# Kernel tuning notes

Measured on AMD Instinct MI355X. Metric: run time of the kernel, lower is better.

Reference implementation:

```python
import jax, jax.numpy as jnp
import numpy as np


def setup_inputs() -> dict:
    key = jax.random.key(0)
    ks = jax.random.split(key, 8)
    B, S, H, I = 2, 1025, 3200, 12800
    T = B * S
    # int8 tensors represented as int32, symmetric range [-128, 126]
    hidden_states = jax.random.randint(ks[0], (B, S, H), 0, 255, dtype=jnp.int32) - 127
    scale_in = (jax.random.uniform(ks[1], (T,)) * 0.02 + 1e-4).astype(jnp.float16)
    w1 = jax.random.randint(ks[2], (I, H), 0, 255, dtype=jnp.int32) - 127
    w1_scale = (jax.random.uniform(ks[3], (I,)) * 0.01 + 1e-4).astype(jnp.float32)
    b1 = (jax.random.normal(ks[4], (I,)) * 0.02).astype(jnp.float16)
    w2 = jax.random.randint(ks[5], (H, I), 0, 255, dtype=jnp.int32) - 127
    w2_scale = (jax.random.uniform(ks[6], (H,)) * 0.01 + 1e-4).astype(jnp.float32)
    b2 = (jax.random.normal(ks[7], (H,)) * 0.02).astype(jnp.float16)
    return {"hidden_states": hidden_states, "scale_in": scale_in,
            "w1": w1, "w1_scale": w1_scale, "b1": b1,
            "w2": w2, "w2_scale": w2_scale, "b2": b2}


def _w8a8_linear(x_int, scale_x, w_int, w_scale, bias):
    # int8 GEMM with int32 accumulation, dequant with per-token * per-channel scales
    acc = jnp.matmul(x_int, w_int.T)  # [T, out] int32
    out = acc.astype(jnp.float32) * scale_x[:, None].astype(jnp.float32) * w_scale[None, :]
    return (out + bias.astype(jnp.float32)).astype(jnp.float16)


def _gelu_and_quant(x_f16):
    # fused GELU + per-token dynamic symmetric int8 quantization
    g = jax.nn.gelu(x_f16.astype(jnp.float32), approximate=False)  # [T, I]
    amax = jnp.max(jnp.abs(g), axis=-1)                              # [T]
    scale_act = (amax / 127.0).astype(jnp.float16)
    s = jnp.maximum(scale_act.astype(jnp.float32), 1e-8)
    q = jnp.clip(jnp.round(g / s[:, None]), -128, 127).astype(jnp.int32)
    return q, scale_act


def reference(hidden_states, scale_in, w1, w1_scale, b1, w2, w2_scale, b2):
    B, S, H = hidden_states.shape
    x = hidden_states.reshape(-1, H)               # [T, H] int
    fc1_out = _w8a8_linear(x, scale_in, w1, w1_scale, b1)      # [T, I] fp16
    act_out, scale_act = _gelu_and_quant(fc1_out)              # int8-as-int32, [T] fp16
    fc2_out = _w8a8_linear(act_out, scale_act, w2, w2_scale, b2)  # [T, H] fp16
    return fc2_out
```

## Files before the change

### kernel.cpp

```cpp
#include <hip/hip_runtime.h>
#include <hip/hip_fp16.h>

typedef int v4i __attribute__((ext_vector_type(4)));

#define AS1C(p) ((const __attribute__((address_space(1))) void*)(p))
#define AS3(p)  ((__attribute__((address_space(3))) void*)(p))
#define BARRIER() do { __builtin_amdgcn_s_barrier(); asm volatile("" ::: "memory"); } while (0)

template <int EPI, int BM>
__launch_bounds__(256, 2)
__global__ void gemm_p2(const signed char* __restrict__ A, const signed char* __restrict__ Bw,
                        int M, int N, int K,
                        const float* __restrict__ scale_tok, const float* __restrict__ wsc,
                        const float* __restrict__ bias,
                        __half* __restrict__ gout, unsigned int* __restrict__ amax,
                        float* __restrict__ fout) {
  constexpr int ACH = BM / 16;
  constexpr int CT  = ACH + 16;
  constexpr int CPW = CT / 4;
  constexpr int MI  = BM / 32;
  constexpr int TB  = CT * 1024;
  __shared__ __align__(16) char smem[3 * TB];

  const int tid = threadIdx.x;
  const int lane = tid & 63, wave = tid >> 6;
  const int wavem = wave >> 1, waven = wave & 1;

  const int gy = gridDim.y;
  int lid;
  {
    const int o = blockIdx.y * gridDim.x + blockIdx.x;
    const int nwg = gridDim.x * gy;
    const int q = nwg >> 3, r = nwg & 7;
    const int x = o & 7, p = o >> 3;
    lid = (x < r ? x * (q + 1) : r * (q + 1) + (x - r) * q) + p;
  }
  const long long t0 = (long long)(lid % gy) * BM;
  const long long n0 = (long long)(lid / gy) * 256;
  const int nk = K >> 6;

  const signed char* sp[CPW];
  int dst[CPW];
#pragma unroll
  for (int i = 0; i < CPW; ++i) {
    const int c = wave * CPW + i;
    const bool isA = c < ACH;
    const int lr = (isA ? c : c - ACH) * 16 + (lane >> 2);
    const int gslot = (((lane & 3) ^ ((lr >> 1) & 3)) << 4);
    long long gr = isA ? (t0 + lr) : (n0 + lr);
    const long long rmax = (isA ? (long long)M : (long long)N) - 1;
    if (gr > rmax) gr = rmax;
    sp[i] = (isA ? A : Bw) + gr * (long long)K + gslot;
    dst[i] = c * 1024;
  }

#define STAGE(bi) do { \
    _Pragma("unroll") \
    for (int i = 0; i < CPW; ++i) { \
      __builtin_amdgcn_global_load_lds(AS1C(sp[i]), AS3(&smem[(bi) * TB + dst[i]]), 16, 0, 0); \
      sp[i] += 64; \
    } \
  } while (0)

  const int lh = lane & 15;
  const int xs = (((lane >> 4) ^ ((lh >> 1) & 3)) << 4);
  const int offA = wavem * (BM / 2) * 64 + lh * 64 + xs;
  const int offB = ACH * 1024 + waven * 8192 + lh * 64 + xs;

  v4i acc[MI][8] = {};
  v4i a_[MI], b_[8];

  STAGE(0);
  if (nk > 1) {
    STAGE(1);
    if constexpr (CPW == 6) asm volatile("s_waitcnt vmcnt(6)" ::: "memory");
    else                    asm volatile("s_waitcnt vmcnt(5)" ::: "memory");
  } else {
    asm volatile("s_waitcnt vmcnt(0)" ::: "memory");
  }
  BARRIER();

  int cur = 0;
  for (int t = 0; t < nk; ++t) {
    const char* base = &smem[cur * TB];
    int b2 = cur + 2; if (b2 >= 3) b2 -= 3;
    const bool pf = (t + 2) < nk;

    if (pf) STAGE(b2);
#pragma unroll
    for (int mi = 0; mi < MI; ++mi) a_[mi] = *(const v4i*)(base + offA + mi * 1024);
#pragma unroll
    for (int ni = 0; ni < 8; ++ni) b_[ni] = *(const v4i*)(base + offB + ni * 1024);
#pragma unroll
    for (int mi = 0; mi < MI; ++mi)
#pragma unroll
      for (int ni = 0; ni < 8; ++ni)
        acc[mi][ni] = __builtin_amdgcn_mfma_i32_16x16x64_i8(a_[mi], b_[ni], acc[mi][ni], 0, 0, 0);

    asm volatile("s_waitcnt lgkmcnt(0)" ::: "memory");
    if (pf) {
      if constexpr (CPW == 6) asm volatile("s_waitcnt vmcnt(6)" ::: "memory");
      else                    asm volatile("s_waitcnt vmcnt(5)" ::: "memory");
    } else {
      asm volatile("s_waitcnt vmcnt(0)" ::: "memory");
    }
    BARRIER();
    cur += 1; if (cur >= 3) cur = 0;
  }
#undef STAGE

  long long cidx[8]; float w8[8], bi8[8]; bool cok[8];
#pragma unroll
  for (int ni = 0; ni < 8; ++ni) {
    cidx[ni] = n0 + waven * 128 + ni * 16 + lh;
    cok[ni] = cidx[ni] < N;
    w8[ni] = cok[ni] ? wsc[cidx[ni]] : 0.f;
    bi8[ni] = cok[ni] ? bias[cidx[ni]] : 0.f;
  }
  if (EPI == 0) {
#pragma unroll
    for (int mi = 0; mi < MI; ++mi) {
#pragma unroll
      for (int j = 0; j < 4; ++j) {
        const long long t = t0 + wavem * (BM / 2) + mi * 16 + (lane >> 4) * 4 + j;
        const bool valid = t < M;
        const float st = valid ? scale_tok[t] : 0.f;
        float rowmax = 0.f;
#pragma unroll
        for (int ni = 0; ni < 8; ++ni) {
          float v = (float)acc[mi][ni][j] * st * w8[ni] + bi8[ni];
          v = __half2float(__float2half(v));
          const float gl = 0.5f * v * (1.f + erff(v * 0.70710678118654752f));
          rowmax = fmaxf(rowmax, fabsf(gl));
          if (valid && cok[ni]) gout[t * (long long)N + cidx[ni]] = __float2half(gl);
        }
#pragma unroll
        for (int m = 1; m < 16; m <<= 1) rowmax = fmaxf(rowmax, __shfl_xor(rowmax, m));
        if (valid && lh == 0) atomicMax(&amax[t], __float_as_uint(rowmax));
      }
    }
  } else {
#pragma unroll
    for (int mi = 0; mi < MI; ++mi) {
#pragma unroll
      for (int j = 0; j < 4; ++j) {
        const long long t = t0 + wavem * (BM / 2) + mi * 16 + (lane >> 4) * 4 + j;
        if (t < M) {
          const float am = __uint_as_float(amax[t]);
          const float st = __half2float(__float2half(am * (1.f / 127.f)));
#pragma unroll
          for (int ni = 0; ni < 8; ++ni) {
            const float v = (float)acc[mi][ni][j] * st * w8[ni] + bi8[ni];
            if (cok[ni]) fout[t * (long long)N + cidx[ni]] = __half2float(__float2half(v));
          }
        }
      }
    }
  }
}

__global__ void pack_all(const int* __restrict__ a, const int* __restrict__ b,
                         const int* __restrict__ c,
                         signed char* __restrict__ pa, signed char* __restrict__ pb,
                         signed char* __restrict__ pc,
                         unsigned int* __restrict__ amax,
                         long long na, long long nb, long long nc, int T) {
  const long long gid = blockIdx.x * (long long)blockDim.x + threadIdx.x;
  if (gid < T) amax[gid] = 0u;
  const long long n4a = na >> 2, n4b = nb >> 2, n4c = nc >> 2;
  const long long tot = n4a + n4b + n4c;
  const long long stride = (long long)gridDim.x * blockDim.x;
  for (long long u = gid; u < tot; u += stride) {
    const int* src; signed char* dst; long long loc;
    if (u < n4a)            { src = a; dst = pa; loc = u; }
    else if (u < n4a + n4b) { src = b; dst = pb; loc = u - n4a; }
    else                    { src = c; dst = pc; loc = u - n4a - n4b; }
    const int4 v = *(const int4*)(src + (loc << 2));
    const unsigned out = (unsigned)(v.x & 0xff) | ((unsigned)(v.y & 0xff) << 8) |
                         ((unsigned)(v.z & 0xff) << 16) | ((unsigned)(v.w & 0xff) << 24);
    *(unsigned*)(dst + (loc << 2)) = out;
  }
}

__global__ void gelu_quant(const __half* __restrict__ g, const unsigned int* __restrict__ amax,
                           signed char* __restrict__ q, long long total, int I) {
  const long long nchunk = total >> 3;
  const long long stride = (long long)gridDim.x * blockDim.x;
  for (long long c = blockIdx.x * (long long)blockDim.x + threadIdx.x; c < nchunk; c += stride) {
    const long long base = c << 3;
    const int t = (int)(base / I);
    const float am = __uint_as_float(amax[t]);
    const float s = fmaxf(__half2float(__float2half(am * (1.f / 127.f))), 1e-8f);
    const float inv = 1.f / s;
    const int4 raw = *(const int4*)(g + base);
    const __half2* h2 = (const __half2*)&raw;
    union { signed char b[8]; int2 v; } u;
#pragma unroll
    for (int k = 0; k < 4; ++k) {
      const float2 f = __half22float2(h2[k]);
      const float q0 = fminf(fmaxf(rintf(f.x * inv), -128.f), 127.f);
      const float q1 = fminf(fmaxf(rintf(f.y * inv), -128.f), 127.f);
      u.b[k * 2]     = (signed char)(int)q0;
      u.b[k * 2 + 1] = (signed char)(int)q1;
    }
    *(int2*)(q + base) = u.v;
  }
}

extern "C" void kernel_launch(void* const* d_in, const int* in_sizes, int n_in,
                              void* d_out, int out_size, void* d_ws, size_t ws_size,
                              hipStream_t stream) {
  const int* hs = (const int*)d_in[0];
  const float* scale_in = (const float*)d_in[1];
  const int* w1 = (const int*)d_in[2];
  const float* w1s = (const float*)d_in[3];
  const float* b1 = (const float*)d_in[4];
  const int* w2 = (const int*)d_in[5];
  const float* w2s = (const float*)d_in[6];
  const float* b2 = (const float*)d_in[7];

  const int T = in_sizes[1];
  const int I = in_sizes[3];
  const int H = in_sizes[6];

  char* ws = (char*)d_ws;
  unsigned int* amax = (unsigned int*)ws;
  signed char* px  = (signed char*)(ws + 16384);
  signed char* pw1 = px + (size_t)T * H;
  signed char* pw2 = pw1 + (size_t)I * H;
  __half* gbuf = (__half*)(pw2 + (size_t)H * I);
  signed char* qbuf = (signed char*)(gbuf + (size_t)T * I);

  const long long nx = (long long)T * H, nw1 = (long long)I * H, nw2 = (long long)H * I;

  pack_all<<<2048, 256, 0, stream>>>(hs, w1, w2, px, pw1, pw2, amax, nx, nw1, nw2, T);

  dim3 g1(I / 256, (T + 127) / 128);
  gemm_p2<0, 128><<<g1, 256, 0, stream>>>(px, pw1, T, I, H, scale_in, w1s, b1, gbuf, amax, nullptr);

  gelu_quant<<<2048, 256, 0, stream>>>(gbuf, amax, qbuf, (long long)T * I, I);

  dim3 g2((H + 255) / 256, (T + 63) / 64);
  gemm_p2<1, 64><<<g2, 256, 0, stream>>>(qbuf, pw2, T, H, I, nullptr, w2s, b2, nullptr, amax, (float*)d_out);
}
```

Before: 415.2 us.

## Use larger 512-thread GEMM tiles with 4-stage LDS pipeline and MFMA priority

Replaces the 256-thread int8 GEMM with a 512-thread variant (2x4 waves). FC1 moves to 256x256 output tiles and FC2 to 128x256. The LDS ring grows from 3 to 4 stages, with waits and barriers moved to the top of each iteration. A-fragment loads are split in two halves around MFMA bursts raised with s_setprio. The aim is more data reuse per tile and better hiding of load latency. The cost is one workgroup per CU, more LDS and register pressure, and fewer tiles for the small token count (about 9 row tiles for FC1), which may leave CUs idle.

```diff
diff --git a/kernel.cpp b/kernel.cpp
--- a/kernel.cpp
+++ b/kernel.cpp
@@ -8,23 +8,24 @@
 #define BARRIER() do { __builtin_amdgcn_s_barrier(); asm volatile("" ::: "memory"); } while (0)
 
 template <int EPI, int BM>
-__launch_bounds__(256, 2)
-__global__ void gemm_p2(const signed char* __restrict__ A, const signed char* __restrict__ Bw,
-                        int M, int N, int K,
-                        const float* __restrict__ scale_tok, const float* __restrict__ wsc,
-                        const float* __restrict__ bias,
-                        __half* __restrict__ gout, unsigned int* __restrict__ amax,
-                        float* __restrict__ fout) {
+__launch_bounds__(512, 1)
+__global__ void gemm_fat(const signed char* __restrict__ A, const signed char* __restrict__ Bw,
+                         int M, int N, int K,
+                         const float* __restrict__ scale_tok, const float* __restrict__ wsc,
+                         const float* __restrict__ bias,
+                         __half* __restrict__ gout, unsigned int* __restrict__ amax,
+                         float* __restrict__ fout) {
   constexpr int ACH = BM / 16;
   constexpr int CT  = ACH + 16;
-  constexpr int CPW = CT / 4;
+  constexpr int CPW = CT / 8;
+  constexpr int TB  = CT * 1024;
   constexpr int MI  = BM / 32;
-  constexpr int TB  = CT * 1024;
-  __shared__ __align__(16) char smem[3 * TB];
+  constexpr int MH  = MI / 2;
+  __shared__ __align__(16) char smem[4 * TB];
 
   const int tid = threadIdx.x;
   const int lane = tid & 63, wave = tid >> 6;
-  const int wavem = wave >> 1, waven = wave & 1;
+  const int wavem = wave >> 2, waven = wave & 3;
 
   const int gy = gridDim.y;
   int lid;
@@ -65,57 +66,66 @@
   const int lh = lane & 15;
   const int xs = (((lane >> 4) ^ ((lh >> 1) & 3)) << 4);
   const int offA = wavem * (BM / 2) * 64 + lh * 64 + xs;
-  const int offB = ACH * 1024 + waven * 8192 + lh * 64 + xs;
-
-  v4i acc[MI][8] = {};
-  v4i a_[MI], b_[8];
+  const int offB = ACH * 1024 + waven * 4096 + lh * 64 + xs;
+
+  v4i acc[MI][4] = {};
 
   STAGE(0);
-  if (nk > 1) {
-    STAGE(1);
-    if constexpr (CPW == 6) asm volatile("s_waitcnt vmcnt(6)" ::: "memory");
-    else                    asm volatile("s_waitcnt vmcnt(5)" ::: "memory");
-  } else {
-    asm volatile("s_waitcnt vmcnt(0)" ::: "memory");
-  }
-  BARRIER();
+  if (nk > 1) STAGE(1);
+  if (nk > 2) STAGE(2);
 
   int cur = 0;
   for (int t = 0; t < nk; ++t) {
-    const char* base = &smem[cur * TB];
-    int b2 = cur + 2; if (b2 >= 3) b2 -= 3;
-    const bool pf = (t + 2) < nk;
-
-    if (pf) STAGE(b2);
-#pragma unroll
-    for (int mi = 0; mi < MI; ++mi) a_[mi] = *(const v4i*)(base + offA + mi * 1024);
-#pragma unroll
-    for (int ni = 0; ni < 8; ++ni) b_[ni] = *(const v4i*)(base + offB + ni * 1024);
-#pragma unroll
-    for (int mi = 0; mi < MI; ++mi)
-#pragma unroll
-      for (int ni = 0; ni < 8; ++ni)
-        acc[mi][ni] = __builtin_amdgcn_mfma_i32_16x16x64_i8(a_[mi], b_[ni], acc[mi][ni], 0, 0, 0);
-
-    asm volatile("s_waitcnt lgkmcnt(0)" ::: "memory");
-    if (pf) {
-      if constexpr (CPW == 6) asm volatile("s_waitcnt vmcnt(6)" ::: "memory");
-      else                    asm volatile("s_waitcnt vmcnt(5)" ::: "memory");
+    if (t < nk - 2) {
+      if constexpr (CPW == 4) asm volatile("s_waitcnt vmcnt(8)" ::: "memory");
+      else                    asm volatile("s_waitcnt vmcnt(6)" ::: "memory");
+    } else if (t == nk - 2) {
+      if constexpr (CPW == 4) asm volatile("s_waitcnt vmcnt(4)" ::: "memory");
+      else                    asm volatile("s_waitcnt vmcnt(3)" ::: "memory");
     } else {
       asm volatile("s_waitcnt vmcnt(0)" ::: "memory");
     }
     BARRIER();
-    cur += 1; if (cur >= 3) cur = 0;
+
+    const char* base = &smem[cur * TB];
+    if (t + 3 < nk) STAGE((cur + 3) & 3);
+
+    v4i b_[4], a0_[MH], a1_[MH];
+#pragma unroll
+    for (int mi = 0; mi < MH; ++mi) a0_[mi] = *(const v4i*)(base + offA + mi * 1024);
+#pragma unroll
+    for (int ni = 0; ni < 4; ++ni) b_[ni] = *(const v4i*)(base + offB + ni * 1024);
+
+    __builtin_amdgcn_s_setprio(1);
+#pragma unroll
+    for (int mi = 0; mi < MH; ++mi)
+#pragma unroll
+      for (int ni = 0; ni < 4; ++ni)
+        acc[mi][ni] = __builtin_amdgcn_mfma_i32_16x16x64_i8(a0_[mi], b_[ni], acc[mi][ni], 0, 0, 0);
+    __builtin_amdgcn_s_setprio(0);
+
+#pragma unroll
+    for (int mi = 0; mi < MH; ++mi) a1_[mi] = *(const v4i*)(base + offA + (MH + mi) * 1024);
+
+    __builtin_amdgcn_s_setprio(1);
+#pragma unroll
+    for (int mi = 0; mi < MH; ++mi)
+#pragma unroll
+      for (int ni = 0; ni < 4; ++ni)
+        acc[MH + mi][ni] = __builtin_amdgcn_mfma_i32_16x16x64_i8(a1_[mi], b_[ni], acc[MH + mi][ni], 0, 0, 0);
+    __builtin_amdgcn_s_setprio(0);
+
+    cur = (cur + 1) & 3;
   }
 #undef STAGE
 
-  long long cidx[8]; float w8[8], bi8[8]; bool cok[8];
-#pragma unroll
-  for (int ni = 0; ni < 8; ++ni) {
-    cidx[ni] = n0 + waven * 128 + ni * 16 + lh;
+  long long cidx[4]; float w4[4], bi4[4]; bool cok[4];
+#pragma unroll
+  for (int ni = 0; ni < 4; ++ni) {
+    cidx[ni] = n0 + waven * 64 + ni * 16 + lh;
     cok[ni] = cidx[ni] < N;
-    w8[ni] = cok[ni] ? wsc[cidx[ni]] : 0.f;
-    bi8[ni] = cok[ni] ? bias[cidx[ni]] : 0.f;
+    w4[ni] = cok[ni] ? wsc[cidx[ni]] : 0.f;
+    bi4[ni] = cok[ni] ? bias[cidx[ni]] : 0.f;
   }
   if (EPI == 0) {
 #pragma unroll
@@ -127,8 +137,8 @@
         const float st = valid ? scale_tok[t] : 0.f;
         float rowmax = 0.f;
 #pragma unroll
-        for (int ni = 0; ni < 8; ++ni) {
-          float v = (float)acc[mi][ni][j] * st * w8[ni] + bi8[ni];
+        for (int ni = 0; ni < 4; ++ni) {
+          float v = (float)acc[mi][ni][j] * st * w4[ni] + bi4[ni];
           v = __half2float(__float2half(v));
           const float gl = 0.5f * v * (1.f + erff(v * 0.70710678118654752f));
           rowmax = fmaxf(rowmax, fabsf(gl));
@@ -149,8 +159,8 @@
           const float am = __uint_as_float(amax[t]);
           const float st = __half2float(__float2half(am * (1.f / 127.f)));
 #pragma unroll
-          for (int ni = 0; ni < 8; ++ni) {
-            const float v = (float)acc[mi][ni][j] * st * w8[ni] + bi8[ni];
+          for (int ni = 0; ni < 4; ++ni) {
+            const float v = (float)acc[mi][ni][j] * st * w4[ni] + bi4[ni];
             if (cok[ni]) fout[t * (long long)N + cidx[ni]] = __half2float(__float2half(v));
           }
         }
@@ -235,11 +245,11 @@
 
   pack_all<<<2048, 256, 0, stream>>>(hs, w1, w2, px, pw1, pw2, amax, nx, nw1, nw2, T);
 
-  dim3 g1(I / 256, (T + 127) / 128);
-  gemm_p2<0, 128><<<g1, 256, 0, stream>>>(px, pw1, T, I, H, scale_in, w1s, b1, gbuf, amax, nullptr);
+  dim3 g1(I / 256, (T + 255) / 256);
+  gemm_fat<0, 256><<<g1, 512, 0, stream>>>(px, pw1, T, I, H, scale_in, w1s, b1, gbuf, amax, nullptr);
 
   gelu_quant<<<2048, 256, 0, stream>>>(gbuf, amax, qbuf, (long long)T * I, I);
 
-  dim3 g2((H + 255) / 256, (T + 63) / 64);
-  gemm_p2<1, 64><<<g2, 256, 0, stream>>>(qbuf, pw2, T, H, I, nullptr, w2s, b2, nullptr, amax, (float*)d_out);
-}
+  dim3 g2((H + 255) / 256, (T + 127) / 128);
+  gemm_fat<1, 128><<<g2, 512, 0, stream>>>(qbuf, pw2, T, H, I, nullptr, w2s, b2, nullptr, amax, (float*)d_out);
+}
```

After: 374.5 us. -9.8%, faster.
